# Kernel tuning notes

Measured on AMD Instinct MI355X. Metric: run time of the kernel, lower is better.

## Reference

```python
import jax, jax.numpy as jnp
import numpy as np

H = 768


def lstm_cell(x, h, c, Wih, Whh, b):
    # PyTorch LSTMCell gate order: i, f, g, o
    gates = x @ Wih.T + h @ Whh.T + b
    i, f, g, o = jnp.split(gates, 4, axis=-1)
    c = jax.nn.sigmoid(f) * c + jax.nn.sigmoid(i) * jnp.tanh(g)
    h = jax.nn.sigmoid(o) * jnp.tanh(c)
    return h, c


def run_lstm(x, Wih, Whh, b, reverse):
    B = x.shape[0]
    Hd = Whh.shape[1]
    def step(carry, xt):
        h, c = lstm_cell(xt, carry[0], carry[1], Wih, Whh, b)
        return (h, c), h
    init = (jnp.zeros((B, Hd), x.dtype), jnp.zeros((B, Hd), x.dtype))
    _, hs = jax.lax.scan(step, init, jnp.swapaxes(x, 0, 1), reverse=reverse)
    return jnp.swapaxes(hs, 0, 1)


def _forward(hidden_state, golds, lstm_Wih_f, lstm_Whh_f, lstm_b_f,
             lstm_Wih_b, lstm_Whh_b, lstm_b_b, subw_Wih, subw_Whh, subw_b,
             word_Wih, word_Whh, word_b, cls_W, cls_b):
    B, T, _ = hidden_state.shape
    dt = hidden_state.dtype
    out_f = run_lstm(hidden_state, lstm_Wih_f, lstm_Whh_f, lstm_b_f, False)
    out_b = run_lstm(hidden_state, lstm_Wih_b, lstm_Whh_b, lstm_b_b, True)
    lstm_out = jnp.concatenate([out_f, out_b], -1)  # [B, T, 2H]

    subw_map = jnp.array([1, 2, 2], dtype=jnp.int32)
    word_map = jnp.array([0, 1, 1], dtype=jnp.int32)
    bidx = jnp.arange(B)
    S1, S2 = 2 * T + 2, T + 1
    carry0 = (jnp.zeros((S1, B, H), dt), jnp.zeros((S1, B, H), dt), jnp.zeros((B,), jnp.int32),
              jnp.zeros((S2, B, H), dt), jnp.zeros((S2, B, H), dt), jnp.zeros((B,), jnp.int32))
    xs = (jnp.swapaxes(lstm_out[:, :T - 1], 0, 1),  # features for subword cell at step idx-1
          jnp.swapaxes(lstm_out[:, 1:T], 0, 1),     # features concatenated into cls at step idx
          golds[:, 1:T].T.astype(jnp.int32))

    def step(carry, x):
        sh, sc, spos, wh, wc, wpos = carry
        x_prev, x_cur, g = x
        # subword stack-LSTM: read top-of-stack state, push new state at pos+1
        h1, c1 = lstm_cell(x_prev, sh[spos, bidx], sc[spos, bidx], subw_Wih, subw_Whh, subw_b)
        sh = sh.at[spos + 1, bidx].set(h1)
        sc = sc.at[spos + 1, bidx].set(c1)
        subword = jnp.concatenate([h1, c1], -1)  # [B, 2H] input to word stack-LSTM
        # word stack-LSTM
        h2, c2 = lstm_cell(subword, wh[wpos, bidx], wc[wpos, bidx], word_Wih, word_Whh, word_b)
        wh = wh.at[wpos + 1, bidx].set(h2)
        wc = wc.at[wpos + 1, bidx].set(c2)
        out = jnp.concatenate([h2, x_cur], -1) @ cls_W.T + cls_b  # [B, 2]
        # training path: ops from gold actions
        sop = subw_map[g]
        wop = word_map[g]
        spos = jnp.where(sop == 1, spos + 1, 0)      # APP: push; SEP: clear subword stack
        wpos = jnp.where(wop == 1, wpos + 1, wpos)   # SEP: push word; APP: hold
        return (sh, sc, spos, wh, wc, wpos), out

    _, outs = jax.lax.scan(step, carry0, xs)  # [T-1, B, 2]
    pred0 = jnp.broadcast_to(jnp.asarray([-1.0, 1.0], dt), (1, B, 2))
    return jnp.swapaxes(jnp.concatenate([pred0, outs], 0), 0, 1)  # [B, T, 2]


def setup_inputs() -> dict:
    key = jax.random.key(0)
    ks = jax.random.split(key, 12)
    B, T = 64, 256
    s = 0.02
    W = lambda k, shape: jax.random.normal(k, shape, jnp.float32) * s
    return {
        "hidden_state": jax.random.normal(ks[0], (B, T, H), jnp.float32),
        "golds": jax.random.randint(ks[1], (B, T), 0, 2),
        "lstm_Wih_f": W(ks[2], (4 * H, H)), "lstm_Whh_f": W(ks[3], (4 * H, H)), "lstm_b_f": jnp.zeros((4 * H,), jnp.float32),
        "lstm_Wih_b": W(ks[4], (4 * H, H)), "lstm_Whh_b": W(ks[5], (4 * H, H)), "lstm_b_b": jnp.zeros((4 * H,), jnp.float32),
        "subw_Wih": W(ks[6], (4 * H, 2 * H)), "subw_Whh": W(ks[7], (4 * H, H)), "subw_b": jnp.zeros((4 * H,), jnp.float32),
        "word_Wih": W(ks[8], (4 * H, 2 * H)), "word_Whh": W(ks[9], (4 * H, H)), "word_b": jnp.zeros((4 * H,), jnp.float32),
        "cls_W": W(ks[10], (2, 3 * H)), "cls_b": jnp.zeros((2,), jnp.float32),
    }


def reference(hidden_state, golds, lstm_Wih_f, lstm_Whh_f, lstm_b_f,
              lstm_Wih_b, lstm_Whh_b, lstm_b_b, subw_Wih, subw_Whh, subw_b,
              word_Wih, word_Whh, word_b, cls_W, cls_b):
    return _forward(hidden_state, golds, lstm_Wih_f, lstm_Whh_f, lstm_b_f,
                    lstm_Wih_b, lstm_Whh_b, lstm_b_b, subw_Wih, subw_Whh, subw_b,
                    word_Wih, word_Whh, word_b, cls_W, cls_b)
```

## Files before the change

kernel.cpp:

```cpp
#include <hip/hip_runtime.h>
#include <hip/hip_bf16.h>

typedef __attribute__((ext_vector_type(8))) short bf16x8;
typedef __attribute__((ext_vector_type(4))) float f32x4;
typedef __attribute__((ext_vector_type(4))) unsigned u32x4;

#define HD   768
#define NB   64
#define NT   256
#define NGATE 3072
#define FPAD 32

__device__ __forceinline__ float fast_sig(float x) { return 1.f / (1.f + __expf(-x)); }
__device__ __forceinline__ float fast_tanh(float x) {
  float t = __expf(-2.f * fabsf(x));
  float r = (1.f - t) / (1.f + t);
  return x < 0.f ? -r : r;
}
__device__ __forceinline__ float bf2f(unsigned short u) {
  union { unsigned i; float f; } v; v.i = ((unsigned)u) << 16; return v.f;
}
__device__ __forceinline__ unsigned short f2bfu(float f) {
  union { __hip_bfloat16 b; unsigned short u; } c;
  c.b = __float2bfloat16(f);
  return c.u;
}
__device__ __forceinline__ unsigned pack2(float a, float b) {
  return (unsigned)f2bfu(a) | ((unsigned)f2bfu(b) << 16);
}

#define VMW(N) do { asm volatile("s_waitcnt vmcnt(" #N ")" ::: "memory"); \
                    __builtin_amdgcn_sched_barrier(0); } while (0)

__device__ __forceinline__ int aload(int* p) {
  return __hip_atomic_load(p, __ATOMIC_RELAXED, __HIP_MEMORY_SCOPE_AGENT);
}
__device__ __forceinline__ void ustore(unsigned* p, unsigned v) {
  __hip_atomic_store(p, v, __ATOMIC_RELAXED, __HIP_MEMORY_SCOPE_AGENT);
}
__device__ __forceinline__ void ustore64(unsigned long long* p, unsigned long long v) {
  __hip_atomic_store(p, v, __ATOMIC_RELAXED, __HIP_MEMORY_SCOPE_AGENT);
}
__device__ __forceinline__ u32x4 cload16(const char* p) {
  u32x4 r;
  asm volatile("global_load_dwordx4 %0, %1, off sc0 sc1"
               : "=v"(r) : "v"(p) : "memory");
  return r;
}
__device__ __forceinline__ unsigned cload4(const char* p) {
  unsigned r;
  asm volatile("global_load_dword %0, %1, off sc0 sc1"
               : "=v"(r) : "v"(p) : "memory");
  return r;
}

__device__ __forceinline__ void arrive_flag(int* f) {
  asm volatile("s_waitcnt vmcnt(0)" ::: "memory");
  __syncthreads();
  if (threadIdx.x == 0)
    __hip_atomic_fetch_add(f, 1, __ATOMIC_RELAXED, __HIP_MEMORY_SCOPE_AGENT);
}

__device__ __forceinline__ void wait2(int* fa, int ta, int* fb, int tb) {
  int tid = threadIdx.x;
  int* p = nullptr; int tgt = 0;
  if (tid < 96)                            { p = fa + tid * FPAD;         tgt = ta; }
  else if (fb && tid >= 128 && tid < 224)  { p = fb + (tid - 128) * FPAD; tgt = tb; }
  if (p && tgt > 0) {
    int guard = 0;
    while (aload(p) < tgt) {
      __builtin_amdgcn_s_sleep(1);
      if (++guard > (1 << 17)) break;
    }
  }
  __syncthreads();
}

__device__ __forceinline__ void wait_coarse(int* fa, int t) {
  int tid = threadIdx.x;
  if (tid < 96) {
    int guard = 0;
    while (aload(fa + tid * FPAD) < t) {
      __builtin_amdgcn_s_sleep(127);
      if (++guard > (1 << 15)) break;
    }
  }
  __syncthreads();
}

__device__ __forceinline__ int frag_dw(int b, int j) {
  return (((((j >> 5) * 4 + (b >> 4)) * 4 + ((j >> 3) & 3)) * 16 + (b & 15)) * 4)
         + ((j & 7) >> 1);
}

__device__ __forceinline__ int wswz(int r) {
  return ((r & 7) << 4) | (((r >> 3) & 3) << 7);
}

__device__ __forceinline__ void load_W_lds(unsigned short* Wl,
                                           const __hip_bfloat16* Wg,
                                           int n_base, int K)
{
  int chunksPerRow = (K * 2) / 16;
  int total = 32 * chunksPerRow;
  for (int idx = threadIdx.x; idx < total; idx += 256) {
    int r  = idx / chunksPerRow;
    int cb = (idx % chunksPerRow) * 16;
    bf16x8 v = *(const bf16x8*)((const char*)(Wg + (long)(n_base + r) * K) + cb);
    *(bf16x8*)((char*)Wl + (long)r * (K * 2) + (cb ^ wswz(r))) = v;
  }
}

__device__ __forceinline__ void mfma_cached(
    const __hip_bfloat16* a0p, int kbase, int NIT,
    const char* w0, const char* w1, int xr0, int xr1, int kk,
    f32x4& acc0, f32x4& acc1)
{
  #pragma unroll 4
  for (int it = kbase; it < kbase + NIT; ++it) {
    bf16x8 av = *(const bf16x8*)(a0p + it * 32 + kk);
    int oo = (it * 32 + kk) * 2;
    bf16x8 bv0 = *(const bf16x8*)(w0 + (oo ^ xr0));
    bf16x8 bv1 = *(const bf16x8*)(w1 + (oo ^ xr1));
    acc0 = __builtin_amdgcn_mfma_f32_16x16x32_bf16(av, bv0, acc0, 0, 0, 0);
    acc1 = __builtin_amdgcn_mfma_f32_16x16x32_bf16(av, bv1, acc1, 0, 0, 0);
  }
}

template<int CF>
__device__ __forceinline__ void mfma_frag(
    const char* Fbase, int l, int w,
    const char* w0, const char* w1, int xr0, int xr1, int kk, int kbase,
    f32x4& acc0, f32x4& acc1)
{
  const char* fp = Fbase + (size_t)(w * 64 + l) * 16;
  u32x4 st[2][12];
  #pragma unroll
  for (int i = 0; i < 12; ++i)
    st[0][i] = cload16(fp + (size_t)i * 4096);
  #pragma unroll
  for (int c = 0; c < CF / 12; ++c) {
    if (c + 1 < CF / 12) {
      #pragma unroll
      for (int i = 0; i < 12; ++i)
        st[(c + 1) & 1][i] = cload16(fp + (size_t)((c + 1) * 12 + i) * 4096);
      asm volatile("s_waitcnt vmcnt(12)" ::: "memory");
    } else {
      asm volatile("s_waitcnt vmcnt(0)" ::: "memory");
    }
    __builtin_amdgcn_sched_barrier(0);
    #pragma unroll
    for (int i = 0; i < 12; ++i) {
      int oo = ((kbase + c * 12 + i) * 32 + kk) * 2;
      bf16x8 av = __builtin_bit_cast(bf16x8, st[c & 1][i]);
      bf16x8 bv0 = *(const bf16x8*)(w0 + (oo ^ xr0));
      bf16x8 bv1 = *(const bf16x8*)(w1 + (oo ^ xr1));
      acc0 = __builtin_amdgcn_mfma_f32_16x16x32_bf16(av, bv0, acc0, 0, 0, 0);
      acc1 = __builtin_amdgcn_mfma_f32_16x16x32_bf16(av, bv1, acc1, 0, 0, 0);
    }
  }
}

__device__ __forceinline__ void issue12(u32x4* dst, const char* base, int c0) {
  #pragma unroll
  for (int i = 0; i < 12; ++i)
    dst[i] = cload16(base + (size_t)(c0 + i) * 4096);
}

__device__ __forceinline__ void mfma_st12(
    const u32x4* st, int kbase,
    const char* w0, const char* w1, int xr0, int xr1, int kk,
    f32x4& acc0, f32x4& acc1)
{
  #pragma unroll
  for (int i = 0; i < 12; ++i) {
    int oo = ((kbase + i) * 32 + kk) * 2;
    bf16x8 av = __builtin_bit_cast(bf16x8, st[i]);
    bf16x8 bv0 = *(const bf16x8*)(w0 + (oo ^ xr0));
    bf16x8 bv1 = *(const bf16x8*)(w1 + (oo ^ xr1));
    acc0 = __builtin_amdgcn_mfma_f32_16x16x32_bf16(av, bv0, acc0, 0, 0, 0);
    acc1 = __builtin_amdgcn_mfma_f32_16x16x32_bf16(av, bv1, acc1, 0, 0, 0);
  }
}

__device__ __forceinline__ void pack_seg(const float* Wih, const float* Whh,
                                         __hip_bfloat16* dst, int Kih,
                                         long id0, long stride)
{
  int K = Kih + HD;
  long total = (long)NGATE * K;
  for (long idx = id0; idx < total; idx += stride) {
    int np = (int)(idx / K), k = (int)(idx % K);
    int j = np >> 2, g = np & 3;
    int n = g * HD + j;
    float v = (k < Kih) ? Wih[(long)n * Kih + k] : Whh[(long)n * HD + (k - Kih)];
    dst[idx] = __float2bfloat16(v);
  }
}

__global__ void setup_kernel(
    const float* __restrict__ x,
    const float* __restrict__ WihF, const float* __restrict__ WhhF,
    const float* __restrict__ WihB, const float* __restrict__ WhhB,
    const float* __restrict__ WihS, const float* __restrict__ WhhS,
    const float* __restrict__ WihW, const float* __restrict__ WhhW,
    __hip_bfloat16* __restrict__ X16,
    __hip_bfloat16* __restrict__ WF, __hip_bfloat16* __restrict__ WB,
    __hip_bfloat16* __restrict__ WS, __hip_bfloat16* __restrict__ WW)
{
  long id0 = (long)blockIdx.x * blockDim.x + threadIdx.x;
  long stride = (long)gridDim.x * blockDim.x;
  for (long i = id0; i < (long)NB * NT * HD; i += stride)
    X16[i] = __float2bfloat16(x[i]);
  pack_seg(WihF, WhhF, WF, 768, id0, stride);
  pack_seg(WihB, WhhB, WB, 768, id0, stride);
  pack_seg(WihS, WhhS, WS, 1536, id0, stride);
  pack_seg(WihW, WhhW, WW, 1536, id0, stride);
}

__global__ void fill_sentinel(float* out, int n, float v)
{
  int i = blockIdx.x * blockDim.x + threadIdx.x;
  if (i < n) out[i] = v;
}

__global__ __launch_bounds__(256, 1) void bilstm_persist(
    const __hip_bfloat16* __restrict__ X16,
    const __hip_bfloat16* __restrict__ WF,
    const __hip_bfloat16* __restrict__ WB,
    const float* __restrict__ bF, const float* __restrict__ bB,
    unsigned* __restrict__ H16u,
    __hip_bfloat16* __restrict__ L16,
    int* __restrict__ flags)
{
  __shared__ unsigned short Wl[32 * 1536];
  __shared__ float gl[64][33];
  int blk = blockIdx.x, dir = blk / 96, nt = blk % 96;
  load_W_lds(Wl, dir ? WB : WF, nt * 32, 1536);
  const float* bias = dir ? bB : bF;
  int* myflags = flags + dir * 96 * FPAD;
  int tid = threadIdx.x;
  unsigned* L16u = (unsigned*)L16;

  int w = tid >> 6, l = tid & 63, lr = l & 15, lh = l >> 4;
  const char* w0 = (const char*)Wl + lr * 3072;
  const char* w1 = (const char*)Wl + (16 + lr) * 3072;
  int xr0 = wswz(lr), xr1 = wswz(16 + lr);
  int kk = 8 * lh;
  int bA = 16 * w + lr;

  int e0 = tid * 2;
  int b = e0 >> 3, jj = e0 & 7;
  int j0 = nt * 8 + jj;
  float bv[2][4];
  #pragma unroll
  for (int u = 0; u < 2; ++u) {
    bv[u][0] = bias[j0 + u];          bv[u][1] = bias[HD + j0 + u];
    bv[u][2] = bias[2 * HD + j0 + u]; bv[u][3] = bias[3 * HD + j0 + u];
  }
  int fdw = frag_dw(b, j0);
  float cst[2] = {0.f, 0.f};
  __syncthreads();

  for (int s = 0; s < NT; ++s) {
    int par = s & 1;
    int t = dir ? (NT - 1 - s) : s;
    f32x4 acc0 = {0.f, 0.f, 0.f, 0.f};
    f32x4 acc1 = {0.f, 0.f, 0.f, 0.f};
    mfma_cached(X16 + (long)t * HD + (long)bA * (NT * HD), 0, 24,
                w0, w1, xr0, xr1, kk, acc0, acc1);
    if (s > 0) wait2(myflags, s, nullptr, 0);
    mfma_frag<24>((const char*)(H16u + (long)(par * 2 + dir) * 24576),
                  l, w, w0, w1, xr0, xr1, kk, 24, acc0, acc1);
    #pragma unroll
    for (int r = 0; r < 4; ++r) {
      gl[16 * w + 4 * lh + r][lr]      = acc0[r];
      gl[16 * w + 4 * lh + r][16 + lr] = acc1[r];
    }
    __syncthreads();
    float hv[2];
    #pragma unroll
    for (int u = 0; u < 2; ++u) {
      int col = 4 * (jj + u);
      float vi = gl[b][col + 0] + bv[u][0];
      float vf = gl[b][col + 1] + bv[u][1];
      float vg = gl[b][col + 2] + bv[u][2];
      float vo = gl[b][col + 3] + bv[u][3];
      float si = fast_sig(vi), sf = fast_sig(vf), so = fast_sig(vo);
      float tg = fast_tanh(vg);
      float c = sf * cst[u] + si * tg;
      cst[u] = c;
      hv[u] = so * fast_tanh(c);
    }
    unsigned pk = pack2(hv[0], hv[1]);
    ustore(H16u + (long)((par ^ 1) * 2 + dir) * 24576 + fdw, pk);
    L16u[((long)b * NT + t) * 768 + dir * 384 + (j0 >> 1)] = pk;
    if (s < NT - 1) arrive_flag(myflags + nt * FPAD);
  }
}

__global__ __launch_bounds__(256, 1) void stack_persist(
    const __hip_bfloat16* __restrict__ L16,
    const __hip_bfloat16* __restrict__ WS,
    const __hip_bfloat16* __restrict__ WW,
    const float* __restrict__ bS, const float* __restrict__ bW,
    const int* __restrict__ golds,
    const float* __restrict__ clsW, const float* __restrict__ clsb,
    unsigned* __restrict__ H1Su,
    unsigned* __restrict__ H2Su,
    unsigned* __restrict__ SUBWu,
    float* __restrict__ OUTC,
    float* __restrict__ out,
    int* __restrict__ flags)
{
  __shared__ unsigned short Wl[32 * 2304];
  __shared__ float gl[64][33];
  int blk = blockIdx.x, role = blk / 96, nt = blk % 96;
  int* flagS = flags + 2 * 96 * FPAD;
  int* flagW = flags + 3 * 96 * FPAD;
  int tid = threadIdx.x;

  if (role == 2) {
    int q = blk - 192;
    int b = tid >> 2, o = (tid >> 1) & 1, hh = tid & 1;
    #pragma unroll
    for (int i = 0; i < 4; ++i) {
      int t = q * 4 + i;
      if (t == 0) {
        if (hh == 0) out[((long)b * NT) * 2 + o] = o ? 1.f : -1.f;
      } else {
        const bf16x8* xp = (const bf16x8*)(L16 + ((long)b * NT + t) * 1536 + hh * 768);
        const float* wv = clsW + o * 2304 + HD + hh * 768;
        float s = 0.f;
        for (int k = 0; k < 96; ++k) {
          bf16x8 v = xp[k];
          #pragma unroll
          for (int e = 0; e < 8; ++e)
            s += bf2f((unsigned short)v[e]) * wv[k * 8 + e];
        }
        s += __shfl_down(s, 1);
        if (hh == 0) out[((long)b * NT + t) * 2 + o] = s + clsb[o];
      }
    }
    for (int i = 0; i < 4; ++i) {
      int t = q * 4 + i;
      if (t < 1) continue;
      int sstep = t - 1;
      wait_coarse(flagW, t);
      if (tid < 128) {
        const char* bp = (const char*)OUTC + (((size_t)sstep * 96) * 128 + tid) * 4;
        float acc = 0.f;
        unsigned bufA[12], bufB[12];
        #pragma unroll
        for (int k = 0; k < 12; ++k) bufA[k] = cload4(bp + (size_t)k * 512);
        #pragma unroll
        for (int c = 0; c < 8; ++c) {
          if (c + 1 < 8) {
            if ((c & 1) == 0) {
              #pragma unroll
              for (int k = 0; k < 12; ++k)
                bufB[k] = cload4(bp + (size_t)((c + 1) * 12 + k) * 512);
            } else {
              #pragma unroll
              for (int k = 0; k < 12; ++k)
                bufA[k] = cload4(bp + (size_t)((c + 1) * 12 + k) * 512);
            }
            VMW(12);
          } else {
            VMW(0);
          }
          if ((c & 1) == 0) {
            #pragma unroll
            for (int k = 0; k < 12; ++k) acc += __builtin_bit_cast(float, bufA[k]);
          } else {
            #pragma unroll
            for (int k = 0; k < 12; ++k) acc += __builtin_bit_cast(float, bufB[k]);
          }
        }
        out[((long)(tid >> 1) * NT + t) * 2 + (tid & 1)] += acc;
      }
    }
    return;
  }

  const float* bias = role ? bW : bS;
  load_W_lds(Wl, role ? WW : WS, nt * 32, 2304);

  int w = tid >> 6, l = tid & 63, lr = l & 15, lh = l >> 4;
  const char* w0 = (const char*)Wl + lr * 4608;
  const char* w1 = (const char*)Wl + (16 + lr) * 4608;
  int xr0 = wswz(lr), xr1 = wswz(16 + lr);
  int kk = 8 * lh;
  int bA = 16 * w + lr;

  int e0 = tid * 2;
  int b = e0 >> 3, jj = e0 & 7;
  int j0 = nt * 8 + jj;
  float bv[2][4];
  #pragma unroll
  for (int u = 0; u < 2; ++u) {
    bv[u][0] = bias[j0 + u];          bv[u][1] = bias[HD + j0 + u];
    bv[u][2] = bias[2 * HD + j0 + u]; bv[u][3] = bias[3 * HD + j0 + u];
  }
  const int* gp = golds + b * NT + 1;
  int fdw_h = frag_dw(b, j0);
  float cst[2] = {0.f, 0.f};
  float hreg[2] = {0.f, 0.f};
  __syncthreads();

  if (role == 0) {
    int fdw_c = frag_dw(b, 768 + j0);
    for (int s = 0; s < NT - 1; ++s) {
      int g = gp[s];
      const __hip_bfloat16* lb = L16 + (long)s * 1536 + (long)bA * (NT * 1536);
      f32x4 acc0 = {0.f, 0.f, 0.f, 0.f};
      f32x4 acc1 = {0.f, 0.f, 0.f, 0.f};
      mfma_cached(lb, 0, 24, w0, w1, xr0, xr1, kk, acc0, acc1);
      wait2(flagS, s, flagW, s - 3);
      mfma_cached(lb, 24, 24, w0, w1, xr0, xr1, kk, acc0, acc1);
      mfma_frag<24>((const char*)(H1Su + (long)(s & 1) * 24576),
                    l, w, w0, w1, xr0, xr1, kk, 48, acc0, acc1);
      #pragma unroll
      for (int r = 0; r < 4; ++r) {
        gl[16 * w + 4 * lh + r][lr]      = acc0[r];
        gl[16 * w + 4 * lh + r][16 + lr] = acc1[r];
      }
      __syncthreads();
      float h1v[2], c1v[2];
      #pragma unroll
      for (int u = 0; u < 2; ++u) {
        int col = 4 * (jj + u);
        float vi = gl[b][col + 0] + bv[u][0];
        float vf = gl[b][col + 1] + bv[u][1];
        float vg = gl[b][col + 2] + bv[u][2];
        float vo = gl[b][col + 3] + bv[u][3];
        float si = fast_sig(vi), sf = fast_sig(vf), so = fast_sig(vo);
        float tg = fast_tanh(vg);
        c1v[u] = sf * cst[u] + si * tg;
        h1v[u] = so * fast_tanh(c1v[u]);
      }
      bool push = (g == 0);
      unsigned pkh = pack2(h1v[0], h1v[1]);
      unsigned pkc = pack2(c1v[0], c1v[1]);
      unsigned* sb = SUBWu + (long)(s & 3) * 49152;
      ustore(sb + fdw_h, pkh);
      ustore(sb + fdw_c, pkc);
      ustore(H1Su + (long)((s + 1) & 1) * 24576 + fdw_h, push ? pkh : 0u);
      cst[0] = push ? c1v[0] : 0.f;
      cst[1] = push ? c1v[1] : 0.f;
      arrive_flag(flagS + nt * FPAD);
    }
  } else {
    float cw0[2], cw1[2];
    #pragma unroll
    for (int u = 0; u < 2; ++u) { cw0[u] = clsW[j0 + u]; cw1[u] = clsW[2304 + j0 + u]; }
    for (int s = 0; s < NT - 1; ++s) {
      int g = gp[s];
      wait2(flagW, s, nullptr, 0);
      const char* fpH = (const char*)(H2Su + (long)(s & 1) * 24576)
                        + (size_t)(w * 64 + l) * 16;
      const char* fpS = (const char*)(SUBWu + (long)(s & 3) * 49152)
                        + (size_t)(w * 64 + l) * 16;
      u32x4 sA[12], sB[12], sC[12];
      issue12(sA, fpH, 0);
      issue12(sB, fpH, 12);
      wait2(flagS, s + 1, nullptr, 0);
      issue12(sC, fpS, 0);
      f32x4 acc0 = {0.f, 0.f, 0.f, 0.f};
      f32x4 acc1 = {0.f, 0.f, 0.f, 0.f};
      VMW(24);
      mfma_st12(sA, 48, w0, w1, xr0, xr1, kk, acc0, acc1);
      issue12(sA, fpS, 12);
      VMW(24);
      mfma_st12(sB, 60, w0, w1, xr0, xr1, kk, acc0, acc1);
      issue12(sB, fpS, 24);
      VMW(24);
      mfma_st12(sC, 0, w0, w1, xr0, xr1, kk, acc0, acc1);
      issue12(sC, fpS, 36);
      VMW(24);
      mfma_st12(sA, 12, w0, w1, xr0, xr1, kk, acc0, acc1);
      VMW(12);
      mfma_st12(sB, 24, w0, w1, xr0, xr1, kk, acc0, acc1);
      VMW(0);
      mfma_st12(sC, 36, w0, w1, xr0, xr1, kk, acc0, acc1);
      #pragma unroll
      for (int r = 0; r < 4; ++r) {
        gl[16 * w + 4 * lh + r][lr]      = acc0[r];
        gl[16 * w + 4 * lh + r][16 + lr] = acc1[r];
      }
      __syncthreads();
      float p0 = 0.f, p1 = 0.f;
      float h2v[2], c2v[2];
      #pragma unroll
      for (int u = 0; u < 2; ++u) {
        int col = 4 * (jj + u);
        float vi = gl[b][col + 0] + bv[u][0];
        float vf = gl[b][col + 1] + bv[u][1];
        float vg = gl[b][col + 2] + bv[u][2];
        float vo = gl[b][col + 3] + bv[u][3];
        float si = fast_sig(vi), sf = fast_sig(vf), so = fast_sig(vo);
        float tg = fast_tanh(vg);
        c2v[u] = sf * cst[u] + si * tg;
        h2v[u] = so * fast_tanh(c2v[u]);
        p0 += h2v[u] * cw0[u];
        p1 += h2v[u] * cw1[u];
      }
      bool push = (g >= 1);
      #pragma unroll
      for (int u = 0; u < 2; ++u) {
        cst[u]  = push ? c2v[u] : cst[u];
        hreg[u] = push ? h2v[u] : hreg[u];
      }
      ustore(H2Su + (long)((s + 1) & 1) * 24576 + fdw_h, pack2(hreg[0], hreg[1]));
      p0 += __shfl_down(p0, 1); p1 += __shfl_down(p1, 1);
      p0 += __shfl_down(p0, 2); p1 += __shfl_down(p1, 2);
      if ((tid & 3) == 0) {
        int bb = tid >> 2;
        union { float f[2]; unsigned long long u; } pkc;
        pkc.f[0] = p0; pkc.f[1] = p1;
        ustore64((unsigned long long*)&OUTC[(((size_t)s * 96) + nt) * 128 + bb * 2],
                 pkc.u);
      }
      arrive_flag(flagW + nt * FPAD);
    }
  }
}

extern "C" void kernel_launch(void* const* d_in, const int* in_sizes, int n_in,
                              void* d_out, int out_size, void* d_ws, size_t ws_size,
                              hipStream_t stream)
{
  const float* x     = (const float*)d_in[0];
  const int*   golds = (const int*)d_in[1];
  const float* WihF  = (const float*)d_in[2];
  const float* WhhF  = (const float*)d_in[3];
  const float* bF    = (const float*)d_in[4];
  const float* WihB  = (const float*)d_in[5];
  const float* WhhB  = (const float*)d_in[6];
  const float* bB    = (const float*)d_in[7];
  const float* WihS  = (const float*)d_in[8];
  const float* WhhS  = (const float*)d_in[9];
  const float* bS    = (const float*)d_in[10];
  const float* WihW  = (const float*)d_in[11];
  const float* WhhW  = (const float*)d_in[12];
  const float* bW    = (const float*)d_in[13];
  const float* clsW  = (const float*)d_in[14];
  const float* clsb  = (const float*)d_in[15];
  float* out = (float*)d_out;

  const size_t OFF_X16  = 0;
  const size_t OFF_WF   = 25165824;
  const size_t OFF_WB   = 34603008;
  const size_t OFF_WS   = 44040192;
  const size_t OFF_WW   = 58195968;
  const size_t OFF_L16  = 72351744;
  const size_t OFF_H16  = 122683392;
  const size_t OFF_H1S  = 123076608;
  const size_t OFF_H2S  = 123273216;
  const size_t OFF_SUBW = 123469824;
  const size_t OFF_FLG  = 124256256;
  const size_t WS_NEEDED = 124305408;

  if (ws_size < WS_NEEDED) {
    fill_sentinel<<<(out_size + 255) / 256, 256, 0, stream>>>(out, out_size, 12345.f);
    return;
  }

  char* ws = (char*)d_ws;
  __hip_bfloat16* X16  = (__hip_bfloat16*)(ws + OFF_X16);
  __hip_bfloat16* WF   = (__hip_bfloat16*)(ws + OFF_WF);
  __hip_bfloat16* WB   = (__hip_bfloat16*)(ws + OFF_WB);
  __hip_bfloat16* WSp  = (__hip_bfloat16*)(ws + OFF_WS);
  __hip_bfloat16* WWp  = (__hip_bfloat16*)(ws + OFF_WW);
  __hip_bfloat16* L16  = (__hip_bfloat16*)(ws + OFF_L16);
  unsigned*       H16u = (unsigned*)(ws + OFF_H16);
  unsigned*       H1Su = (unsigned*)(ws + OFF_H1S);
  unsigned*       H2Su = (unsigned*)(ws + OFF_H2S);
  unsigned*       SUBWu= (unsigned*)(ws + OFF_SUBW);
  float*          OUTC = (float*)(ws + OFF_X16);
  int*            flags= (int*)(ws + OFF_FLG);

  setup_kernel<<<4096, 256, 0, stream>>>(x, WihF, WhhF, WihB, WhhB,
                                         WihS, WhhS, WihW, WhhW,
                                         X16, WF, WB, WSp, WWp);
  hipMemsetAsync(ws + OFF_H16, 0, WS_NEEDED - OFF_H16, stream);

  bilstm_persist<<<192, 256, 0, stream>>>(X16, WF, WB, bF, bB, H16u, L16, flags);

  stack_persist<<<256, 256, 0, stream>>>(L16, WSp, WWp, bS, bW, golds,
                                         clsW, clsb, H1Su, H2Su, SUBWu,
                                         OUTC, out, flags);
}
```

Baseline: 3.884 ms.

## Replace cache-bypassing fragment loads with cache invalidation plus plain cached loads

Cross-block state fragments were previously read with sc0 sc1 loads that bypass the caches, software-pipelined in batches of 12. These are replaced by a single buffer_inv after each flag wait followed by ordinary cached loads in a simple unrolled loop. The word role now waits on both flags at once before loading, and the subword role moves all of its L16 input MFMAs ahead of the wait. The classifier role now splits work across two half-blocks combined through shared memory and writes its outputs with atomic stores, where it previously used a read-modify-write. The invalidate flushes the whole L1 every step and the manual load/MFMA overlap is gone, so latency hiding now depends on the compiler.

```diff
diff --git a/kernel.cpp b/kernel.cpp
--- a/kernel.cpp
+++ b/kernel.cpp
@@ -32,6 +32,10 @@
 #define VMW(N) do { asm volatile("s_waitcnt vmcnt(" #N ")" ::: "memory"); \
                     __builtin_amdgcn_sched_barrier(0); } while (0)
 
+#define INVALL() do { \
+  asm volatile("s_waitcnt vmcnt(0)\n\tbuffer_inv sc0 sc1" ::: "memory"); \
+  __builtin_amdgcn_sched_barrier(0); } while (0)
+
 __device__ __forceinline__ int aload(int* p) {
   return __hip_atomic_load(p, __ATOMIC_RELAXED, __HIP_MEMORY_SCOPE_AGENT);
 }
@@ -41,11 +45,9 @@
 __device__ __forceinline__ void ustore64(unsigned long long* p, unsigned long long v) {
   __hip_atomic_store(p, v, __ATOMIC_RELAXED, __HIP_MEMORY_SCOPE_AGENT);
 }
-__device__ __forceinline__ u32x4 cload16(const char* p) {
-  u32x4 r;
-  asm volatile("global_load_dwordx4 %0, %1, off sc0 sc1"
-               : "=v"(r) : "v"(p) : "memory");
-  return r;
+__device__ __forceinline__ void fstore(float* p, float v) {
+  __hip_atomic_store((unsigned*)p, __builtin_bit_cast(unsigned, v),
+                     __ATOMIC_RELAXED, __HIP_MEMORY_SCOPE_AGENT);
 }
 __device__ __forceinline__ unsigned cload4(const char* p) {
   unsigned r;
@@ -128,54 +130,16 @@
 }
 
 template<int CF>
-__device__ __forceinline__ void mfma_frag(
+__device__ __forceinline__ void mfma_fragp(
     const char* Fbase, int l, int w,
     const char* w0, const char* w1, int xr0, int xr1, int kk, int kbase,
     f32x4& acc0, f32x4& acc1)
 {
   const char* fp = Fbase + (size_t)(w * 64 + l) * 16;
-  u32x4 st[2][12];
-  #pragma unroll
-  for (int i = 0; i < 12; ++i)
-    st[0][i] = cload16(fp + (size_t)i * 4096);
-  #pragma unroll
-  for (int c = 0; c < CF / 12; ++c) {
-    if (c + 1 < CF / 12) {
-      #pragma unroll
-      for (int i = 0; i < 12; ++i)
-        st[(c + 1) & 1][i] = cload16(fp + (size_t)((c + 1) * 12 + i) * 4096);
-      asm volatile("s_waitcnt vmcnt(12)" ::: "memory");
-    } else {
-      asm volatile("s_waitcnt vmcnt(0)" ::: "memory");
-    }
-    __builtin_amdgcn_sched_barrier(0);
-    #pragma unroll
-    for (int i = 0; i < 12; ++i) {
-      int oo = ((kbase + c * 12 + i) * 32 + kk) * 2;
-      bf16x8 av = __builtin_bit_cast(bf16x8, st[c & 1][i]);
-      bf16x8 bv0 = *(const bf16x8*)(w0 + (oo ^ xr0));
-      bf16x8 bv1 = *(const bf16x8*)(w1 + (oo ^ xr1));
-      acc0 = __builtin_amdgcn_mfma_f32_16x16x32_bf16(av, bv0, acc0, 0, 0, 0);
-      acc1 = __builtin_amdgcn_mfma_f32_16x16x32_bf16(av, bv1, acc1, 0, 0, 0);
-    }
-  }
-}
-
-__device__ __forceinline__ void issue12(u32x4* dst, const char* base, int c0) {
-  #pragma unroll
-  for (int i = 0; i < 12; ++i)
-    dst[i] = cload16(base + (size_t)(c0 + i) * 4096);
-}
-
-__device__ __forceinline__ void mfma_st12(
-    const u32x4* st, int kbase,
-    const char* w0, const char* w1, int xr0, int xr1, int kk,
-    f32x4& acc0, f32x4& acc1)
-{
-  #pragma unroll
-  for (int i = 0; i < 12; ++i) {
-    int oo = ((kbase + i) * 32 + kk) * 2;
-    bf16x8 av = __builtin_bit_cast(bf16x8, st[i]);
+  #pragma unroll 4
+  for (int it = 0; it < CF; ++it) {
+    bf16x8 av = *(const bf16x8*)(fp + (size_t)it * 4096);
+    int oo = ((kbase + it) * 32 + kk) * 2;
     bf16x8 bv0 = *(const bf16x8*)(w0 + (oo ^ xr0));
     bf16x8 bv1 = *(const bf16x8*)(w1 + (oo ^ xr1));
     acc0 = __builtin_amdgcn_mfma_f32_16x16x32_bf16(av, bv0, acc0, 0, 0, 0);
@@ -270,8 +234,9 @@
     mfma_cached(X16 + (long)t * HD + (long)bA * (NT * HD), 0, 24,
                 w0, w1, xr0, xr1, kk, acc0, acc1);
     if (s > 0) wait2(myflags, s, nullptr, 0);
-    mfma_frag<24>((const char*)(H16u + (long)(par * 2 + dir) * 24576),
-                  l, w, w0, w1, xr0, xr1, kk, 24, acc0, acc1);
+    INVALL();
+    mfma_fragp<24>((const char*)(H16u + (long)(par * 2 + dir) * 24576),
+                   l, w, w0, w1, xr0, xr1, kk, 24, acc0, acc1);
     #pragma unroll
     for (int r = 0; r < 4; ++r) {
       gl[16 * w + 4 * lh + r][lr]      = acc0[r];
@@ -294,7 +259,7 @@
     }
     unsigned pk = pack2(hv[0], hv[1]);
     ustore(H16u + (long)((par ^ 1) * 2 + dir) * 24576 + fdw, pk);
-    L16u[((long)b * NT + t) * 768 + dir * 384 + (j0 >> 1)] = pk;
+    ustore(L16u + ((long)b * NT + t) * 768 + dir * 384 + (j0 >> 1), pk);
     if (s < NT - 1) arrive_flag(myflags + nt * FPAD);
   }
 }
@@ -321,16 +286,20 @@
   int tid = threadIdx.x;
 
   if (role == 2) {
+    __shared__ float partial[128];
     int q = blk - 192;
-    int b = tid >> 2, o = (tid >> 1) & 1, hh = tid & 1;
+    int idx = tid & 127;
+    int b = idx >> 1, o = idx & 1;
+    int half = tid >> 7;
+    float clsv[4];
     #pragma unroll
     for (int i = 0; i < 4; ++i) {
       int t = q * 4 + i;
       if (t == 0) {
-        if (hh == 0) out[((long)b * NT) * 2 + o] = o ? 1.f : -1.f;
+        clsv[i] = o ? 1.f : -1.f;
       } else {
-        const bf16x8* xp = (const bf16x8*)(L16 + ((long)b * NT + t) * 1536 + hh * 768);
-        const float* wv = clsW + o * 2304 + HD + hh * 768;
+        const bf16x8* xp = (const bf16x8*)(L16 + ((long)b * NT + t) * 1536 + half * 768);
+        const float* wv = clsW + o * 2304 + HD + half * 768;
         float s = 0.f;
         for (int k = 0; k < 96; ++k) {
           bf16x8 v = xp[k];
@@ -338,18 +307,22 @@
           for (int e = 0; e < 8; ++e)
             s += bf2f((unsigned short)v[e]) * wv[k * 8 + e];
         }
-        s += __shfl_down(s, 1);
-        if (hh == 0) out[((long)b * NT + t) * 2 + o] = s + clsb[o];
+        if (half) partial[idx] = s;
+        __syncthreads();
+        clsv[i] = (half == 0) ? (s + partial[idx] + clsb[o]) : 0.f;
+        __syncthreads();
       }
     }
     for (int i = 0; i < 4; ++i) {
       int t = q * 4 + i;
-      if (t < 1) continue;
-      int sstep = t - 1;
+      if (t == 0) {
+        if (half == 0) fstore(&out[((long)b * NT) * 2 + o], clsv[i]);
+        continue;
+      }
       wait_coarse(flagW, t);
       if (tid < 128) {
-        const char* bp = (const char*)OUTC + (((size_t)sstep * 96) * 128 + tid) * 4;
-        float acc = 0.f;
+        const char* bp = (const char*)OUTC + (((size_t)(t - 1) * 96) * 128 + idx) * 4;
+        float acc = clsv[i];
         unsigned bufA[12], bufB[12];
         #pragma unroll
         for (int k = 0; k < 12; ++k) bufA[k] = cload4(bp + (size_t)k * 512);
@@ -377,7 +350,7 @@
             for (int k = 0; k < 12; ++k) acc += __builtin_bit_cast(float, bufB[k]);
           }
         }
-        out[((long)(tid >> 1) * NT + t) * 2 + (tid & 1)] += acc;
+        fstore(&out[((long)b * NT + t) * 2 + o], acc);
       }
     }
     return;
@@ -415,11 +388,11 @@
       const __hip_bfloat16* lb = L16 + (long)s * 1536 + (long)bA * (NT * 1536);
       f32x4 acc0 = {0.f, 0.f, 0.f, 0.f};
       f32x4 acc1 = {0.f, 0.f, 0.f, 0.f};
-      mfma_cached(lb, 0, 24, w0, w1, xr0, xr1, kk, acc0, acc1);
+      mfma_cached(lb, 0, 48, w0, w1, xr0, xr1, kk, acc0, acc1);
       wait2(flagS, s, flagW, s - 3);
-      mfma_cached(lb, 24, 24, w0, w1, xr0, xr1, kk, acc0, acc1);
-      mfma_frag<24>((const char*)(H1Su + (long)(s & 1) * 24576),
-                    l, w, w0, w1, xr0, xr1, kk, 48, acc0, acc1);
+      INVALL();
+      mfma_fragp<24>((const char*)(H1Su + (long)(s & 1) * 24576),
+                     l, w, w0, w1, xr0, xr1, kk, 48, acc0, acc1);
       #pragma unroll
       for (int r = 0; r < 4; ++r) {
         gl[16 * w + 4 * lh + r][lr]      = acc0[r];
@@ -456,33 +429,14 @@
     for (int u = 0; u < 2; ++u) { cw0[u] = clsW[j0 + u]; cw1[u] = clsW[2304 + j0 + u]; }
     for (int s = 0; s < NT - 1; ++s) {
       int g = gp[s];
-      wait2(flagW, s, nullptr, 0);
-      const char* fpH = (const char*)(H2Su + (long)(s & 1) * 24576)
-                        + (size_t)(w * 64 + l) * 16;
-      const char* fpS = (const char*)(SUBWu + (long)(s & 3) * 49152)
-                        + (size_t)(w * 64 + l) * 16;
-      u32x4 sA[12], sB[12], sC[12];
-      issue12(sA, fpH, 0);
-      issue12(sB, fpH, 12);
-      wait2(flagS, s + 1, nullptr, 0);
-      issue12(sC, fpS, 0);
+      wait2(flagS, s + 1, flagW, s);
+      INVALL();
       f32x4 acc0 = {0.f, 0.f, 0.f, 0.f};
       f32x4 acc1 = {0.f, 0.f, 0.f, 0.f};
-      VMW(24);
-      mfma_st12(sA, 48, w0, w1, xr0, xr1, kk, acc0, acc1);
-      issue12(sA, fpS, 12);
-      VMW(24);
-      mfma_st12(sB, 60, w0, w1, xr0, xr1, kk, acc0, acc1);
-      issue12(sB, fpS, 24);
-      VMW(24);
-      mfma_st12(sC, 0, w0, w1, xr0, xr1, kk, acc0, acc1);
-      issue12(sC, fpS, 36);
-      VMW(24);
-      mfma_st12(sA, 12, w0, w1, xr0, xr1, kk, acc0, acc1);
-      VMW(12);
-      mfma_st12(sB, 24, w0, w1, xr0, xr1, kk, acc0, acc1);
-      VMW(0);
-      mfma_st12(sC, 36, w0, w1, xr0, xr1, kk, acc0, acc1);
+      mfma_fragp<48>((const char*)(SUBWu + (long)(s & 3) * 49152),
+                     l, w, w0, w1, xr0, xr1, kk, 0, acc0, acc1);
+      mfma_fragp<24>((const char*)(H2Su + (long)(s & 1) * 24576),
+                     l, w, w0, w1, xr0, xr1, kk, 48, acc0, acc1);
       #pragma unroll
       for (int r = 0; r < 4; ++r) {
         gl[16 * w + 4 * lh + r][lr]      = acc0[r];
```

Result: slower. 6.946 ms (+78.8%).
